# Kernel optimization log

Hardware: AMD Instinct MI355X
Metric: run time of the kernel (lower is better)

Reference implementation:

```python
import jax, jax.numpy as jnp
import numpy as np

INV_SQRT2 = 0.7071067811865476  # db1 (Haar) filter coefficient
KEYS = ("aad", "ada", "add", "daa", "dad", "dda", "ddd")  # ptwt wavedec3 detail keys, dims (D,H,W)


def dwt1(x, axis):
    """Single-level 1D Haar DWT along `axis` (zero mode, even length -> no padding).
    lo[k] = (x[2k] + x[2k+1]) / sqrt(2), hi[k] = (x[2k] - x[2k+1]) / sqrt(2),
    matching pywt/ptwt db1 with mode='zero'."""
    ev = jax.lax.slice_in_dim(x, 0, None, stride=2, axis=axis)
    od = jax.lax.slice_in_dim(x, 1, None, stride=2, axis=axis)
    return (ev + od) * INV_SQRT2, (ev - od) * INV_SQRT2


def haar3(x):
    """One level of separable 3D Haar DWT on [B, C, D, H, W] -> dict of 8 subbands,
    each [B, C, D/2, H/2, W/2]. Key letters correspond to (D, H, W)."""
    out = {}
    aD, dD = dwt1(x, 2)
    for k0, t0 in (("a", aD), ("d", dD)):
        aH, dH = dwt1(t0, 3)
        for k1, t1 in (("a", aH), ("d", dH)):
            aW, dW = dwt1(t1, 4)
            out[k0 + k1 + "a"] = aW
            out[k0 + k1 + "d"] = dW
    return out


def wavedec3(x, level):
    """Multi-level 3D Haar wavedec (ptwt.wavedec3, wavelet='db1', mode='zero').
    Returns (Yl, [details_coarsest, ..., details_finest])."""
    details = []
    cur = x
    for _ in range(level):
        sb = haar3(cur)
        cur = sb.pop("aaa")
        details.append(sb)
    return cur, details[::-1]  # ptwt orders coarsest level first


def setup_inputs() -> dict:
    key = jax.random.key(0)
    x = jax.random.normal(key, (4, 8, 128, 128, 128), dtype=jnp.float32)
    return {"x": x, "level": 5}


def reference(x, level):
    Yl, Yh = wavedec3(x, level)
    outs = [Yl]
    for d in Yh:
        outs.extend(d[k] for k in KEYS)
    return tuple(outs)
```

## Files before the change

kernel.cpp:

```cpp
#include <hip/hip_runtime.h>


#define C3 0.3535533905932738f

typedef float f4 __attribute__((ext_vector_type(4)));

__global__ __launch_bounds__(256) void haar3_lvl(
    const float* __restrict__ in, float* __restrict__ out_a,
    float* __restrict__ out_d, long det_sz, int log2n, long nq)
{
    const long q = (long)blockIdx.x * 256 + threadIdx.x;
    if (q >= nq) return;
    const int n = 1 << log2n;
    const int wg = (int)(q & ((n >> 2) - 1));
    const int hy = (int)((q >> (log2n - 2)) & (n - 1));
    const int dz = (int)((q >> (2 * log2n - 2)) & (n - 1));
    const long b = q >> (3 * log2n - 2);
    const long n2   = 2 * (long)n;
    const long rowD = n2 * n2;
    const long base = ((b * n2 + 2 * dz) * n2 + 2 * hy) * n2 + 8 * (long)wg;

    __attribute__((aligned(16))) float r[4][8];
    const f4* p00 = (const f4*)(in + base);
    const f4* p01 = (const f4*)(in + base + n2);
    const f4* p10 = (const f4*)(in + base + rowD);
    const f4* p11 = (const f4*)(in + base + rowD + n2);
    *(f4*)&r[0][0] = __builtin_nontemporal_load(p00);
    *(f4*)&r[0][4] = __builtin_nontemporal_load(p00 + 1);
    *(f4*)&r[1][0] = __builtin_nontemporal_load(p01);
    *(f4*)&r[1][4] = __builtin_nontemporal_load(p01 + 1);
    *(f4*)&r[2][0] = __builtin_nontemporal_load(p10);
    *(f4*)&r[2][4] = __builtin_nontemporal_load(p10 + 1);
    *(f4*)&r[3][0] = __builtin_nontemporal_load(p11);
    *(f4*)&r[3][4] = __builtin_nontemporal_load(p11 + 1);

    __attribute__((aligned(16))) float o[8][4];
#pragma unroll
    for (int j = 0; j < 4; ++j) {
        const float aw0 = r[0][2*j] + r[0][2*j+1], dw0 = r[0][2*j] - r[0][2*j+1];
        const float aw1 = r[1][2*j] + r[1][2*j+1], dw1 = r[1][2*j] - r[1][2*j+1];
        const float aw2 = r[2][2*j] + r[2][2*j+1], dw2 = r[2][2*j] - r[2][2*j+1];
        const float aw3 = r[3][2*j] + r[3][2*j+1], dw3 = r[3][2*j] - r[3][2*j+1];
        const float aa0 = aw0 + aw1, da0 = aw0 - aw1, ad0 = dw0 + dw1, dd0 = dw0 - dw1;
        const float aa1 = aw2 + aw3, da1 = aw2 - aw3, ad1 = dw2 + dw3, dd1 = dw2 - dw3;
        o[0][j] = (aa0 + aa1) * C3;
        o[1][j] = (ad0 + ad1) * C3;
        o[2][j] = (da0 + da1) * C3;
        o[3][j] = (dd0 + dd1) * C3;
        o[4][j] = (aa0 - aa1) * C3;
        o[5][j] = (ad0 - ad1) * C3;
        o[6][j] = (da0 - da1) * C3;
        o[7][j] = (dd0 - dd1) * C3;
    }

    const long t4 = q << 2;
    *(f4*)(out_a + t4) = *(const f4*)&o[0][0];
#pragma unroll
    for (int s = 0; s < 7; ++s)
        __builtin_nontemporal_store(*(const f4*)&o[s + 1][0],
                                    (f4*)(out_d + (long)s * det_sz + t4));
}

extern "C" void kernel_launch(void* const* d_in, const int* in_sizes, int n_in,
                              void* d_out, int out_size, void* d_ws, size_t ws_size,
                              hipStream_t stream) {
    const float* x = (const float*)d_in[0];
    float* out  = (float*)d_out;
    float* buf0 = (float*)d_ws;
    float* buf1 = buf0 + 8388608;

    struct Lv { const float* in; float* oa; float* od; int log2n; };
    const Lv lv[5] = {
        { x,    buf0, out + 8388608, 6 },
        { buf0, buf1, out + 1048576, 5 },
        { buf1, buf0, out + 131072,  4 },
        { buf0, buf1, out + 16384,   3 },
        { buf1, out,  out + 2048,    2 },
    };
    const long BC = 32;
    for (int i = 0; i < 5; ++i) {
        const long total = BC << (3 * lv[i].log2n);
        const long nq    = total >> 2;
        const int blocks = (int)((nq + 255) / 256);
        haar3_lvl<<<blocks, 256, 0, stream>>>(lv[i].in, lv[i].oa, lv[i].od,
                                              total, lv[i].log2n, nq);
    }
}
```

Before: 452.0 us.

## Fuse all five Haar levels into one kernel using LDS intermediates

Replaces five per-level launches with one kernel. Each block handles a 32x32x128 input slab, computes level 1 from global memory and keeps the approximation band in shared memory. Levels 2-5 are then computed from LDS with barriers in between. This removes the workspace round trips for the approximation bands and the extra launches, at the cost of a small grid (512 blocks), high LDS usage that limits occupancy, and mostly idle threads at the coarse levels.

```diff
diff --git a/kernel.cpp b/kernel.cpp
--- a/kernel.cpp
+++ b/kernel.cpp
@@ -5,36 +5,14 @@
 
 typedef float f4 __attribute__((ext_vector_type(4)));
 
-__global__ __launch_bounds__(256) void haar3_lvl(
-    const float* __restrict__ in, float* __restrict__ out_a,
-    float* __restrict__ out_d, long det_sz, int log2n, long nq)
-{
-    const long q = (long)blockIdx.x * 256 + threadIdx.x;
-    if (q >= nq) return;
-    const int n = 1 << log2n;
-    const int wg = (int)(q & ((n >> 2) - 1));
-    const int hy = (int)((q >> (log2n - 2)) & (n - 1));
-    const int dz = (int)((q >> (2 * log2n - 2)) & (n - 1));
-    const long b = q >> (3 * log2n - 2);
-    const long n2   = 2 * (long)n;
-    const long rowD = n2 * n2;
-    const long base = ((b * n2 + 2 * dz) * n2 + 2 * hy) * n2 + 8 * (long)wg;
+__device__ __forceinline__ f4 ntload(const float* p) {
+    return __builtin_nontemporal_load((const f4*)p);
+}
+__device__ __forceinline__ void ntstore(float* p, f4 v) {
+    __builtin_nontemporal_store(v, (f4*)p);
+}
 
-    __attribute__((aligned(16))) float r[4][8];
-    const f4* p00 = (const f4*)(in + base);
-    const f4* p01 = (const f4*)(in + base + n2);
-    const f4* p10 = (const f4*)(in + base + rowD);
-    const f4* p11 = (const f4*)(in + base + rowD + n2);
-    *(f4*)&r[0][0] = __builtin_nontemporal_load(p00);
-    *(f4*)&r[0][4] = __builtin_nontemporal_load(p00 + 1);
-    *(f4*)&r[1][0] = __builtin_nontemporal_load(p01);
-    *(f4*)&r[1][4] = __builtin_nontemporal_load(p01 + 1);
-    *(f4*)&r[2][0] = __builtin_nontemporal_load(p10);
-    *(f4*)&r[2][4] = __builtin_nontemporal_load(p10 + 1);
-    *(f4*)&r[3][0] = __builtin_nontemporal_load(p11);
-    *(f4*)&r[3][4] = __builtin_nontemporal_load(p11 + 1);
-
-    __attribute__((aligned(16))) float o[8][4];
+__device__ __forceinline__ void haar_quad(const float r[4][8], float o[8][4]) {
 #pragma unroll
     for (int j = 0; j < 4; ++j) {
         const float aw0 = r[0][2*j] + r[0][2*j+1], dw0 = r[0][2*j] - r[0][2*j+1];
@@ -52,37 +30,123 @@
         o[6][j] = (da0 - da1) * C3;
         o[7][j] = (dd0 - dd1) * C3;
     }
+}
 
-    const long t4 = q << 2;
-    *(f4*)(out_a + t4) = *(const f4*)&o[0][0];
+__device__ __forceinline__ void lds_quad(const float* p, int dh, int dd, float r[4][8]) {
+    *(f4*)&r[0][0] = *(const f4*)(p);
+    *(f4*)&r[0][4] = *(const f4*)(p + 4);
+    *(f4*)&r[1][0] = *(const f4*)(p + dh);
+    *(f4*)&r[1][4] = *(const f4*)(p + dh + 4);
+    *(f4*)&r[2][0] = *(const f4*)(p + dd);
+    *(f4*)&r[2][4] = *(const f4*)(p + dd + 4);
+    *(f4*)&r[3][0] = *(const f4*)(p + dd + dh);
+    *(f4*)&r[3][4] = *(const f4*)(p + dd + dh + 4);
+}
+
+__global__ __launch_bounds__(512, 4) void haar3_fused(
+    const float* __restrict__ in, float* __restrict__ out)
+{
+    __shared__ float A1[16 * 16 * 68];
+    __shared__ float A2[8 * 8 * 36];
+    __shared__ float A3[4 * 4 * 16];
+    __shared__ float A4[2 * 2 * 8];
+
+    const int tid = threadIdx.x;
+    const int bc = blockIdx.x >> 4;
+    const int db = (blockIdx.x >> 2) & 3;
+    const int hb = blockIdx.x & 3;
+
+    const float* xin = in + (((long)bc * 128 + db * 32) * 128 + hb * 32) * 128;
+    float* const d1 = out + 8388608;
+    float* const d2 = out + 1048576;
+    float* const d3 = out + 131072;
+    float* const d4 = out + 16384;
+    float* const d5 = out + 2048;
+
+    for (int it = 0; it < 8; ++it) {
+        const int u = it * 512 + tid;
+        const int wg = u & 15, hy = (u >> 4) & 15, dz = u >> 8;
+        const float* p = xin + ((long)(2 * dz) * 128 + 2 * hy) * 128 + 8 * wg;
+        float r[4][8];
+        *(f4*)&r[0][0] = ntload(p);
+        *(f4*)&r[0][4] = ntload(p + 4);
+        *(f4*)&r[1][0] = ntload(p + 128);
+        *(f4*)&r[1][4] = ntload(p + 132);
+        *(f4*)&r[2][0] = ntload(p + 16384);
+        *(f4*)&r[2][4] = ntload(p + 16388);
+        *(f4*)&r[3][0] = ntload(p + 16512);
+        *(f4*)&r[3][4] = ntload(p + 16516);
+        float o[8][4];
+        haar_quad(r, o);
+        *(f4*)&A1[(dz * 16 + hy) * 68 + 4 * wg] = *(const f4*)&o[0][0];
+        const long di = (((long)bc * 64 + db * 16 + dz) * 64 + hb * 16 + hy) * 64 + 4 * wg;
 #pragma unroll
-    for (int s = 0; s < 7; ++s)
-        __builtin_nontemporal_store(*(const f4*)&o[s + 1][0],
-                                    (f4*)(out_d + (long)s * det_sz + t4));
+        for (int s = 0; s < 7; ++s)
+            ntstore(d1 + (long)s * 8388608 + di, *(const f4*)&o[s + 1][0]);
+    }
+    __syncthreads();
+
+    {
+        const int wg = tid & 7, hy = (tid >> 3) & 7, dz = tid >> 6;
+        float r[4][8];
+        lds_quad(&A1[((2 * dz) * 16 + 2 * hy) * 68 + 8 * wg], 68, 16 * 68, r);
+        float o[8][4];
+        haar_quad(r, o);
+        *(f4*)&A2[(dz * 8 + hy) * 36 + 4 * wg] = *(const f4*)&o[0][0];
+        const long di = (((long)bc * 32 + db * 8 + dz) * 32 + hb * 8 + hy) * 32 + 4 * wg;
+#pragma unroll
+        for (int s = 0; s < 7; ++s)
+            ntstore(d2 + (long)s * 1048576 + di, *(const f4*)&o[s + 1][0]);
+    }
+    __syncthreads();
+
+    if (tid < 64) {
+        const int wg = tid & 3, hy = (tid >> 2) & 3, dz = tid >> 4;
+        float r[4][8];
+        lds_quad(&A2[((2 * dz) * 8 + 2 * hy) * 36 + 8 * wg], 36, 8 * 36, r);
+        float o[8][4];
+        haar_quad(r, o);
+        *(f4*)&A3[(dz * 4 + hy) * 16 + 4 * wg] = *(const f4*)&o[0][0];
+        const long di = (((long)bc * 16 + db * 4 + dz) * 16 + hb * 4 + hy) * 16 + 4 * wg;
+#pragma unroll
+        for (int s = 0; s < 7; ++s)
+            ntstore(d3 + (long)s * 131072 + di, *(const f4*)&o[s + 1][0]);
+    }
+    __syncthreads();
+
+    if (tid < 8) {
+        const int wg = tid & 1, hy = (tid >> 1) & 1, dz = tid >> 2;
+        float r[4][8];
+        lds_quad(&A3[((2 * dz) * 4 + 2 * hy) * 16 + 8 * wg], 16, 64, r);
+        float o[8][4];
+        haar_quad(r, o);
+        *(f4*)&A4[(dz * 2 + hy) * 8 + 4 * wg] = *(const f4*)&o[0][0];
+        const long di = (((long)bc * 8 + db * 2 + dz) * 8 + hb * 2 + hy) * 8 + 4 * wg;
+#pragma unroll
+        for (int s = 0; s < 7; ++s)
+            ntstore(d4 + (long)s * 16384 + di, *(const f4*)&o[s + 1][0]);
+    }
+    __syncthreads();
+
+    if (tid == 0) {
+        float r[4][8];
+        lds_quad(&A4[0], 8, 16, r);
+        float o[8][4];
+        haar_quad(r, o);
+        const long di = (((long)bc * 4 + db) * 4 + hb) * 4;
+        *(f4*)(out + di) = *(const f4*)&o[0][0];
+#pragma unroll
+        for (int s = 0; s < 7; ++s)
+            *(f4*)(d5 + (long)s * 2048 + di) = *(const f4*)&o[s + 1][0];
+    }
 }
 
 extern "C" void kernel_launch(void* const* d_in, const int* in_sizes, int n_in,
                               void* d_out, int out_size, void* d_ws, size_t ws_size,
                               hipStream_t stream) {
     const float* x = (const float*)d_in[0];
-    float* out  = (float*)d_out;
-    float* buf0 = (float*)d_ws;
-    float* buf1 = buf0 + 8388608;
+    float* out = (float*)d_out;
+    (void)d_ws; (void)ws_size;
 
-    struct Lv { const float* in; float* oa; float* od; int log2n; };
-    const Lv lv[5] = {
-        { x,    buf0, out + 8388608, 6 },
-        { buf0, buf1, out + 1048576, 5 },
-        { buf1, buf0, out + 131072,  4 },
-        { buf0, buf1, out + 16384,   3 },
-        { buf1, out,  out + 2048,    2 },
-    };
-    const long BC = 32;
-    for (int i = 0; i < 5; ++i) {
-        const long total = BC << (3 * lv[i].log2n);
-        const long nq    = total >> 2;
-        const int blocks = (int)((nq + 255) / 256);
-        haar3_lvl<<<blocks, 256, 0, stream>>>(lv[i].in, lv[i].oa, lv[i].od,
-                                              total, lv[i].log2n, nq);
-    }
+    haar3_fused<<<512, 512, 0, stream>>>(x, out);
 }
```

After: 456.6 us. No clear change (+1.0%).
